# Performance work log

Hardware: AMD Instinct MI355X
Metric: run time of the kernel (lower is better)

## Reference

```python
import jax, jax.numpy as jnp
import numpy as np

D_MODEL = 1024
D_FF = 4096
NUM_EXPERTS = 8
TOP_K = 2
SEQ = 1024
BATCH = 2


def setup_inputs() -> dict:
    key = jax.random.key(0)
    ks = jax.random.split(key, 7)
    s = 0.02
    x = jax.random.normal(ks[0], (SEQ, BATCH, D_MODEL), dtype=jnp.float32)
    gate_w = jax.random.normal(ks[1], (D_MODEL, NUM_EXPERTS), dtype=jnp.float32) * s
    gate_b = jnp.zeros((NUM_EXPERTS,), dtype=jnp.float32)
    W1 = jax.random.normal(ks[2], (NUM_EXPERTS, D_MODEL, D_FF), dtype=jnp.float32) * s
    b1 = jnp.zeros((NUM_EXPERTS, D_FF), dtype=jnp.float32)
    W2 = jax.random.normal(ks[3], (NUM_EXPERTS, D_FF, D_MODEL), dtype=jnp.float32) * s
    b2 = jnp.zeros((NUM_EXPERTS, D_MODEL), dtype=jnp.float32)
    return {"x": x, "gate_w": gate_w, "gate_b": gate_b,
            "W1": W1, "b1": b1, "W2": W2, "b2": b2}


def reference(x, gate_w, gate_b, W1, b1, W2, b2):
    S, B, D = x.shape
    x_flat = x.reshape(-1, D)                       # [T, D], T = S*B
    scores = x_flat @ gate_w + gate_b               # [T, E]
    topk_vals, topk_idx = jax.lax.top_k(scores, TOP_K)   # [T, K]
    topk_probs = jax.nn.softmax(topk_vals, axis=-1)      # [T, K]
    # combine weight per (token, expert): sum of probs over slots routed to e
    one_hot = jax.nn.one_hot(topk_idx, NUM_EXPERTS, dtype=x.dtype)  # [T, K, E]
    combine = jnp.einsum('tk,tke->te', topk_probs, one_hot)         # [T, E]
    # dense per-expert FFN (tokens with combine weight 0 contribute nothing,
    # matching the masked gather/scatter in the torch loop)
    h = jax.nn.relu(jnp.einsum('td,edf->etf', x_flat, W1) + b1[:, None, :])  # [E, T, F]
    y = jnp.einsum('etf,efd->etd', h, W2) + b2[:, None, :]                    # [E, T, D]
    out = jnp.einsum('te,etd->td', combine, y)       # [T, D]
    return out.reshape(S, B, D)
```

## Files before the change

### kernel.cpp

```cpp
#include <hip/hip_runtime.h>
#include <stdint.h>

#define T_TOKENS 2048
#define DM 1024
#define DF 4096
#define NEXP 8
#define NSLOTS (T_TOKENS * 2)

typedef __bf16 bf16x8 __attribute__((ext_vector_type(8)));
typedef float f32x4 __attribute__((ext_vector_type(4)));

__device__ __forceinline__ ushort f2bf(float f) {
    union { float f; uint32_t u; } v; v.f = f;
    uint32_t r = v.u + 0x7FFFu + ((v.u >> 16) & 1u);
    return (ushort)(r >> 16);
}

__device__ __forceinline__ void gload16(const ushort* g, ushort* l) {
    __builtin_amdgcn_global_load_lds(
        (const __attribute__((address_space(1))) uint32_t*)g,
        (__attribute__((address_space(3))) uint32_t*)l,
        16, 0, 0);
}

__global__ void init_cnt(uint32_t* cnt) {
    if (threadIdx.x < NEXP) cnt[threadIdx.x] = 0;
}

__global__ __launch_bounds__(256) void gate_route(
    const float* __restrict__ x, const float* __restrict__ gw,
    const float* __restrict__ gb,
    uint32_t* __restrict__ route, uint32_t* __restrict__ cnt,
    float* __restrict__ prob)
{
    const int w = threadIdx.x >> 6;
    const int lane = threadIdx.x & 63;
    const int t = blockIdx.x * 4 + w;
    float acc[NEXP];
#pragma unroll
    for (int e = 0; e < NEXP; ++e) acc[e] = 0.f;
    const float* xr = x + (size_t)t * DM;
#pragma unroll
    for (int j = 0; j < DM / 64; ++j) {
        const int d = j * 64 + lane;
        const float xv = xr[d];
        const float* g = gw + (size_t)d * NEXP;
#pragma unroll
        for (int e = 0; e < NEXP; ++e) acc[e] += xv * g[e];
    }
#pragma unroll
    for (int e = 0; e < NEXP; ++e) {
#pragma unroll
        for (int off = 32; off > 0; off >>= 1)
            acc[e] += __shfl_xor(acc[e], off);
        acc[e] += gb[e];
    }
    if (lane == 0) {
        int e0 = 0; float v0 = acc[0];
#pragma unroll
        for (int e = 1; e < NEXP; ++e) if (acc[e] > v0) { v0 = acc[e]; e0 = e; }
        int e1 = -1; float v1 = -1e30f;
#pragma unroll
        for (int e = 0; e < NEXP; ++e) if (e != e0 && acc[e] > v1) { v1 = acc[e]; e1 = e; }
        const float ex = expf(v1 - v0);
        const float inv = 1.f / (1.f + ex);
        prob[t * 2 + 0] = inv;
        prob[t * 2 + 1] = ex * inv;
        uint32_t pos = atomicAdd(&cnt[e0], 1u);
        route[e0 * T_TOKENS + pos] = (uint32_t)(t * 2);
        pos = atomicAdd(&cnt[e1], 1u);
        route[e1 * T_TOKENS + pos] = (uint32_t)(t * 2 + 1);
    }
}

__global__ __launch_bounds__(256) void convert_x(const float* __restrict__ x,
                                                 ushort* __restrict__ xb)
{
    const int i = (blockIdx.x * 256 + threadIdx.x) * 4;
    const float4 v = *reinterpret_cast<const float4*>(x + i);
    ushort4 o;
    o.x = f2bf(v.x); o.y = f2bf(v.y); o.z = f2bf(v.z); o.w = f2bf(v.w);
    *reinterpret_cast<ushort4*>(xb + i) = o;
}

template<int K, int N>
__global__ __launch_bounds__(256) void conv_transpose(const float* __restrict__ W,
                                                      ushort* __restrict__ Wb)
{
    const int e  = blockIdx.y;
    const int nt = blockIdx.x % (N / 64);
    const int kt = blockIdx.x / (N / 64);
    const int k0 = kt * 64, n0 = nt * 64;
    __shared__ ushort T[64][80];
    const int t = threadIdx.x;
    const int kr = t >> 4, nc = (t & 15) * 4;
    const float* src = W + ((size_t)e * K + k0 + kr) * N + n0 + nc;
#pragma unroll
    for (int i = 0; i < 4; ++i) {
        const float4 v = *reinterpret_cast<const float4*>(src + (size_t)i * 16 * N);
        T[nc + 0][kr + i * 16] = f2bf(v.x);
        T[nc + 1][kr + i * 16] = f2bf(v.y);
        T[nc + 2][kr + i * 16] = f2bf(v.z);
        T[nc + 3][kr + i * 16] = f2bf(v.w);
    }
    __syncthreads();
    const int r = t >> 2, c0 = t & 3;
    ushort* dst = Wb + ((size_t)e * N + n0 + r) * K + k0;
#pragma unroll
    for (int i = 0; i < 2; ++i) {
        const int c = c0 + i * 4;
        const uint4 v = *reinterpret_cast<const uint4*>(&T[r][c * 8]);
        *reinterpret_cast<uint4*>(dst + c * 8) = v;
    }
}

template<int KD, int ND, bool FIRST, int SPLIT, int NT>
__global__ __launch_bounds__(256, 2) void moe_gemm4(
    const ushort* __restrict__ Abuf,
    const ushort* __restrict__ Wb,
    const float* __restrict__ bias,
    const uint32_t* __restrict__ route,
    const uint32_t* __restrict__ cnt,
    const float* __restrict__ prob,
    ushort* __restrict__ hout,
    float* __restrict__ yout)
{
    const int bx = blockIdx.x;
    const int e  = bx / (16 * NT);
    const int mt = (bx / NT) & 15;
    const int nt = bx % NT;
    const uint32_t cntE = cnt[e];
    const int m0 = mt * 128;
    if ((uint32_t)m0 >= cntE) return;
    const int n0 = nt * 128;
    const int z  = (SPLIT > 1) ? (int)blockIdx.z : 0;
    const int kbeg = z * (KD / SPLIT);
    const int niter = (KD / SPLIT) / 64;

    __shared__ ushort As[2][128 * 64];
    __shared__ ushort Bs[2][128 * 64];
    __shared__ uint32_t s_route[128];

    const int tid = threadIdx.x;
    if (tid < 128) {
        const uint32_t idx = (uint32_t)(m0 + tid);
        s_route[tid] = (idx < cntE) ? route[e * T_TOKENS + idx] : 0xFFFFFFFFu;
    }
    __syncthreads();

    const int w = tid >> 6, l = tid & 63;

    const ushort* asrc[4];
    const ushort* bsrc[4];
#pragma unroll
    for (int i = 0; i < 4; ++i) {
        const int chunk = (w * 4 + i) * 64 + l;
        const int row = chunk >> 3;
        const int c   = chunk & 7;
        const int cs  = c ^ (((row >> 2) & 1) << 1);
        const uint32_t s = s_route[row];
        const size_t ar = (s == 0xFFFFFFFFu) ? 0 : (FIRST ? (size_t)(s >> 1) : (size_t)s);
        asrc[i] = Abuf + ar * KD + cs * 8 + kbeg;
        bsrc[i] = Wb + ((size_t)e * ND + n0 + row) * KD + cs * 8 + kbeg;
    }

    f32x4 acc[4][4];
#pragma unroll
    for (int i = 0; i < 4; ++i)
#pragma unroll
        for (int j = 0; j < 4; ++j) acc[i][j] = (f32x4){0.f, 0.f, 0.f, 0.f};

    const int q = l & 15, g = l >> 4;
    const int wm = w >> 1, wn = w & 1;

    int aoff[4][2], boff[4][2];
#pragma unroll
    for (int mi = 0; mi < 4; ++mi)
#pragma unroll
        for (int ks = 0; ks < 2; ++ks) {
            int row = wm * 64 + mi * 16 + q;
            int b = row * 128 + ks * 64 + g * 16;
            b ^= ((b >> 9) & 1) << 5;
            aoff[mi][ks] = b;
            row = wn * 64 + mi * 16 + q;
            b = row * 128 + ks * 64 + g * 16;
            b ^= ((b >> 9) & 1) << 5;
            boff[mi][ks] = b;
        }

    ushort* const abase0 = &As[0][0];
    ushort* const bbase0 = &Bs[0][0];

#pragma unroll
    for (int i = 0; i < 4; ++i) gload16(asrc[i], abase0 + (w * 4 + i) * 512);
#pragma unroll
    for (int i = 0; i < 4; ++i) gload16(bsrc[i], bbase0 + (w * 4 + i) * 512);

    int cur = 0;
    for (int t = 0; t < niter; ++t) {
        if (t + 1 < niter) {
            ushort* ad = abase0 + (cur ^ 1) * (128 * 64) + (w * 4) * 512;
            ushort* bd = bbase0 + (cur ^ 1) * (128 * 64) + (w * 4) * 512;
            const int k1 = (t + 1) * 64;
#pragma unroll
            for (int i = 0; i < 4; ++i) gload16(asrc[i] + k1, ad + i * 512);
#pragma unroll
            for (int i = 0; i < 4; ++i) gload16(bsrc[i] + k1, bd + i * 512);
            asm volatile("s_waitcnt vmcnt(8)" ::: "memory");
        } else {
            asm volatile("s_waitcnt vmcnt(0)" ::: "memory");
        }
        __builtin_amdgcn_s_barrier();
        __builtin_amdgcn_sched_barrier(0);

        const char* Ab = (const char*)(abase0 + cur * (128 * 64));
        const char* Bb = (const char*)(bbase0 + cur * (128 * 64));
#pragma unroll
        for (int ks = 0; ks < 2; ++ks) {
            bf16x8 af[4], bv[4];
#pragma unroll
            for (int mi = 0; mi < 4; ++mi)
                af[mi] = *reinterpret_cast<const bf16x8*>(Ab + aoff[mi][ks]);
#pragma unroll
            for (int ni = 0; ni < 4; ++ni)
                bv[ni] = *reinterpret_cast<const bf16x8*>(Bb + boff[ni][ks]);
            __builtin_amdgcn_s_setprio(1);
#pragma unroll
            for (int mi = 0; mi < 4; ++mi)
#pragma unroll
                for (int ni = 0; ni < 4; ++ni)
                    acc[mi][ni] = __builtin_amdgcn_mfma_f32_16x16x32_bf16(
                        af[mi], bv[ni], acc[mi][ni], 0, 0, 0);
            __builtin_amdgcn_s_setprio(0);
        }
        __builtin_amdgcn_s_barrier();
        cur ^= 1;
    }

    const float* brow = bias + (size_t)e * ND;
#pragma unroll
    for (int mi = 0; mi < 4; ++mi) {
#pragma unroll
        for (int ni = 0; ni < 4; ++ni) {
            const int gcol = n0 + wn * 64 + ni * 16 + q;
            const float bv = (SPLIT == 1 || z == 0) ? brow[gcol] : 0.f;
#pragma unroll
            for (int j = 0; j < 4; ++j) {
                const int row = wm * 64 + mi * 16 + g * 4 + j;
                if ((uint32_t)(m0 + row) < cntE) {
                    const uint32_t s = s_route[row];
                    float v = acc[mi][ni][j] + bv;
                    if (FIRST) {
                        v = fmaxf(v, 0.f);
                        hout[(size_t)s * ND + gcol] = f2bf(v);
                    } else {
                        yout[((size_t)z * NSLOTS + s) * ND + gcol] = v * prob[s];
                    }
                }
            }
        }
    }
}

__global__ __launch_bounds__(256) void combine2(const float* __restrict__ yc,
                                                float* __restrict__ out)
{
    const int gid = blockIdx.x * 256 + threadIdx.x;
    const int t = gid >> 8;
    const int dq = gid & 255;
    const float4* Y = reinterpret_cast<const float4*>(yc);
    const float4 a = Y[(size_t)(2 * t) * 256 + dq];
    const float4 b = Y[(size_t)(2 * t + 1) * 256 + dq];
    const float4 c = Y[((size_t)NSLOTS + 2 * t) * 256 + dq];
    const float4 d = Y[((size_t)NSLOTS + 2 * t + 1) * 256 + dq];
    const float4 o = { a.x + b.x + c.x + d.x, a.y + b.y + c.y + d.y,
                       a.z + b.z + c.z + d.z, a.w + b.w + c.w + d.w };
    reinterpret_cast<float4*>(out)[gid] = o;
}

template<int KD, int ND, bool FIRST>
__global__ __launch_bounds__(256) void moe_gemm_v1(
    const ushort* __restrict__ Abuf, const float* __restrict__ W,
    const float* __restrict__ bias, const uint32_t* __restrict__ route,
    const uint32_t* __restrict__ cnt, const float* __restrict__ prob,
    ushort* __restrict__ hout, float* __restrict__ yout)
{
    const int e = blockIdx.x >> 4;
    const int mt = blockIdx.x & 15;
    const uint32_t cntE = cnt[e];
    const int m0 = mt * 128;
    if ((uint32_t)m0 >= cntE) return;
    const int n0 = blockIdx.y * 128;
    const int tid = threadIdx.x;
    __shared__ ushort Asm[128][40];
    __shared__ ushort Bsm[128][40];
    __shared__ uint32_t s_route[128];
    if (tid < 128) {
        const uint32_t idx = (uint32_t)(m0 + tid);
        s_route[tid] = (idx < cntE) ? route[e * T_TOKENS + idx] : 0xFFFFFFFFu;
    }
    __syncthreads();
    const int ar = tid >> 1, ah = tid & 1;
    const uint32_t s_a = s_route[ar];
    size_t arow = 0;
    if (s_a != 0xFFFFFFFFu) arow = FIRST ? (size_t)(s_a >> 1) : (size_t)s_a;
    const ushort* asrc = Abuf + arow * KD + ah * 16;
    const int c4 = tid & 31, kq = tid >> 5;
    const float* wbase = W + (size_t)e * KD * ND + (size_t)n0 + (size_t)c4 * 4;
    f32x4 acc[4][4];
#pragma unroll
    for (int i = 0; i < 4; ++i)
#pragma unroll
        for (int j = 0; j < 4; ++j) acc[i][j] = (f32x4){0.f, 0.f, 0.f, 0.f};
    const int lane = tid & 63, wv = tid >> 6;
    const int wm = wv >> 1, wn = wv & 1;
    const int q = lane & 15, g = lane >> 4;
    for (int k0 = 0; k0 < KD; k0 += 32) {
        {
            const uint4* src = reinterpret_cast<const uint4*>(asrc + k0);
            const uint4 v0 = src[0];
            const uint4 v1 = src[1];
            *reinterpret_cast<uint4*>(&Asm[ar][ah * 16]) = v0;
            *reinterpret_cast<uint4*>(&Asm[ar][ah * 16 + 8]) = v1;
        }
        {
            ushort vals[4][4];
#pragma unroll
            for (int r = 0; r < 4; ++r) {
                const float4 v = *reinterpret_cast<const float4*>(
                    wbase + (size_t)(k0 + kq * 4 + r) * ND);
                vals[r][0] = f2bf(v.x); vals[r][1] = f2bf(v.y);
                vals[r][2] = f2bf(v.z); vals[r][3] = f2bf(v.w);
            }
#pragma unroll
            for (int c = 0; c < 4; ++c) {
                const ushort4 o = { vals[0][c], vals[1][c], vals[2][c], vals[3][c] };
                *reinterpret_cast<ushort4*>(&Bsm[c4 * 4 + c][kq * 4]) = o;
            }
        }
        __syncthreads();
        bf16x8 af[4], bfr[4];
#pragma unroll
        for (int mi = 0; mi < 4; ++mi)
            af[mi] = *reinterpret_cast<const bf16x8*>(&Asm[wm * 64 + mi * 16 + q][g * 8]);
#pragma unroll
        for (int ni = 0; ni < 4; ++ni)
            bfr[ni] = *reinterpret_cast<const bf16x8*>(&Bsm[wn * 64 + ni * 16 + q][g * 8]);
#pragma unroll
        for (int mi = 0; mi < 4; ++mi)
#pragma unroll
            for (int ni = 0; ni < 4; ++ni)
                acc[mi][ni] = __builtin_amdgcn_mfma_f32_16x16x32_bf16(
                    af[mi], bfr[ni], acc[mi][ni], 0, 0, 0);
        __syncthreads();
    }
#pragma unroll
    for (int mi = 0; mi < 4; ++mi) {
#pragma unroll
        for (int ni = 0; ni < 4; ++ni) {
            const int gcol = n0 + wn * 64 + ni * 16 + q;
#pragma unroll
            for (int j = 0; j < 4; ++j) {
                const int row = wm * 64 + mi * 16 + g * 4 + j;
                if ((uint32_t)(m0 + row) < cntE) {
                    const uint32_t s = s_route[row];
                    float v = acc[mi][ni][j] + bias[e * ND + gcol];
                    if (FIRST) {
                        v = fmaxf(v, 0.f);
                        hout[(size_t)s * ND + gcol] = f2bf(v);
                    } else {
                        yout[(size_t)s * ND + gcol] = v * prob[s];
                    }
                }
            }
        }
    }
}

__global__ __launch_bounds__(256) void combine1(const float* __restrict__ yc,
                                                float* __restrict__ out)
{
    const int gid = blockIdx.x * 256 + threadIdx.x;
    const int t = gid >> 8;
    const int dq = gid & 255;
    const float4 va = reinterpret_cast<const float4*>(yc)[(size_t)(2 * t) * 256 + dq];
    const float4 vb = reinterpret_cast<const float4*>(yc)[(size_t)(2 * t + 1) * 256 + dq];
    const float4 o = { va.x + vb.x, va.y + vb.y, va.z + vb.z, va.w + vb.w };
    reinterpret_cast<float4*>(out)[gid] = o;
}

extern "C" void kernel_launch(void* const* d_in, const int* in_sizes, int n_in,
                              void* d_out, int out_size, void* d_ws, size_t ws_size,
                              hipStream_t stream)
{
    const float* x  = (const float*)d_in[0];
    const float* gw = (const float*)d_in[1];
    const float* gb = (const float*)d_in[2];
    const float* W1 = (const float*)d_in[3];
    const float* b1 = (const float*)d_in[4];
    const float* W2 = (const float*)d_in[5];
    const float* b2 = (const float*)d_in[6];
    float* out = (float*)d_out;
    char* ws = (char*)d_ws;

    const size_t OFF_XB    = 0;
    const size_t OFF_H     = 4194304;
    const size_t OFF_YC    = 37748736;
    const size_t OFF_ROUTE = 71303168;
    const size_t OFF_CNT   = 71368704;
    const size_t OFF_PROB  = 71368768;
    const size_t OFF_W1B   = 71385152;
    const size_t OFF_W2B   = 138494016;
    const size_t NEED      = 205602880ull;

    if (ws_size >= NEED) {
        ushort*   xb    = (ushort*)(ws + OFF_XB);
        ushort*   h     = (ushort*)(ws + OFF_H);
        float*    yc    = (float*)(ws + OFF_YC);
        uint32_t* route = (uint32_t*)(ws + OFF_ROUTE);
        uint32_t* cnt   = (uint32_t*)(ws + OFF_CNT);
        float*    prob  = (float*)(ws + OFF_PROB);
        ushort*   w1b   = (ushort*)(ws + OFF_W1B);
        ushort*   w2b   = (ushort*)(ws + OFF_W2B);

        hipLaunchKernelGGL(init_cnt, dim3(1), dim3(64), 0, stream, cnt);
        hipLaunchKernelGGL(gate_route, dim3(T_TOKENS / 4), dim3(256), 0, stream,
                           x, gw, gb, route, cnt, prob);
        hipLaunchKernelGGL(convert_x, dim3(T_TOKENS * DM / 1024), dim3(256), 0, stream, x, xb);
        hipLaunchKernelGGL((conv_transpose<DM, DF>), dim3((DM / 64) * (DF / 64), NEXP),
                           dim3(256), 0, stream, W1, w1b);
        hipLaunchKernelGGL((conv_transpose<DF, DM>), dim3((DF / 64) * (DM / 64), NEXP),
                           dim3(256), 0, stream, W2, w2b);
        hipLaunchKernelGGL((moe_gemm4<DM, DF, true, 1, 32>),
                           dim3(NEXP * 16 * 32, 1, 1), dim3(256), 0, stream,
                           xb, w1b, b1, route, cnt, prob, h, (float*)nullptr);
        hipLaunchKernelGGL((moe_gemm4<DF, DM, false, 2, 8>),
                           dim3(NEXP * 16 * 8, 1, 2), dim3(256), 0, stream,
                           h, w2b, b2, route, cnt, prob, (ushort*)nullptr, yc);
        hipLaunchKernelGGL(combine2, dim3(T_TOKENS * DM / 1024), dim3(256), 0, stream, yc, out);
    } else {
        const size_t F_XB = 0, F_H = 4194304, F_YC = 37748736;
        const size_t F_ROUTE = 54525952, F_CNT = 54591488, F_PROB = 54591552;
        ushort*   xb    = (ushort*)(ws + F_XB);
        ushort*   h     = (ushort*)(ws + F_H);
        float*    yc    = (float*)(ws + F_YC);
        uint32_t* route = (uint32_t*)(ws + F_ROUTE);
        uint32_t* cnt   = (uint32_t*)(ws + F_CNT);
        float*    prob  = (float*)(ws + F_PROB);

        hipLaunchKernelGGL(init_cnt, dim3(1), dim3(64), 0, stream, cnt);
        hipLaunchKernelGGL(gate_route, dim3(T_TOKENS / 4), dim3(256), 0, stream,
                           x, gw, gb, route, cnt, prob);
        hipLaunchKernelGGL(convert_x, dim3(T_TOKENS * DM / 1024), dim3(256), 0, stream, x, xb);
        hipLaunchKernelGGL((moe_gemm_v1<DM, DF, true>), dim3(NEXP * 16, DF / 128),
                           dim3(256), 0, stream, xb, W1, b1, route, cnt, prob,
                           h, (float*)nullptr);
        hipLaunchKernelGGL((moe_gemm_v1<DF, DM, false>), dim3(NEXP * 16, DM / 128),
                           dim3(256), 0, stream, h, W2, b2, route, cnt, prob,
                           (ushort*)nullptr, yc);
        hipLaunchKernelGGL(combine1, dim3(T_TOKENS * DM / 1024), dim3(256), 0, stream, yc, out);
    }
}
```

Measured before the change: 334.7 us.

## Halve GEMM K-tile for higher occupancy and use four-way split-K

The MoE GEMM K-tile drops from 64 to 32, halving shared memory per block. The launch bound rises to 4 blocks per SM so more waves can hide load latency. The second GEMM now splits K four ways instead of two, and the combine kernel sums four partial buffers per slot. To fit the larger partial buffer, it reuses the W1 bf16 region, which is dead after the first GEMM. The cost is twice as many barriers per MFMA and twice the partial-sum traffic written and read back.

After: 315.7 us. 5.7% less time.

```diff
diff --git a/kernel.cpp b/kernel.cpp
--- a/kernel.cpp
+++ b/kernel.cpp
@@ -115,7 +115,7 @@
 }
 
 template<int KD, int ND, bool FIRST, int SPLIT, int NT>
-__global__ __launch_bounds__(256, 2) void moe_gemm4(
+__global__ __launch_bounds__(256, 4) void moe_gemm5(
     const ushort* __restrict__ Abuf,
     const ushort* __restrict__ Wb,
     const float* __restrict__ bias,
@@ -135,10 +135,10 @@
     const int n0 = nt * 128;
     const int z  = (SPLIT > 1) ? (int)blockIdx.z : 0;
     const int kbeg = z * (KD / SPLIT);
-    const int niter = (KD / SPLIT) / 64;
-
-    __shared__ ushort As[2][128 * 64];
-    __shared__ ushort Bs[2][128 * 64];
+    const int niter = (KD / SPLIT) / 32;
+
+    __shared__ ushort As[2][128 * 32];
+    __shared__ ushort Bs[2][128 * 32];
     __shared__ uint32_t s_route[128];
 
     const int tid = threadIdx.x;
@@ -150,14 +150,14 @@
 
     const int w = tid >> 6, l = tid & 63;
 
-    const ushort* asrc[4];
-    const ushort* bsrc[4];
-#pragma unroll
-    for (int i = 0; i < 4; ++i) {
-        const int chunk = (w * 4 + i) * 64 + l;
-        const int row = chunk >> 3;
-        const int c   = chunk & 7;
-        const int cs  = c ^ (((row >> 2) & 1) << 1);
+    const ushort* asrc[2];
+    const ushort* bsrc[2];
+#pragma unroll
+    for (int i = 0; i < 2; ++i) {
+        const int chunk = (w * 2 + i) * 64 + l;
+        const int row = chunk >> 2;
+        const int c   = chunk & 3;
+        const int cs  = c ^ ((row >> 1) & 3);
         const uint32_t s = s_route[row];
         const size_t ar = (s == 0xFFFFFFFFu) ? 0 : (FIRST ? (size_t)(s >> 1) : (size_t)s);
         asrc[i] = Abuf + ar * KD + cs * 8 + kbeg;
@@ -173,66 +173,57 @@
     const int q = l & 15, g = l >> 4;
     const int wm = w >> 1, wn = w & 1;
 
-    int aoff[4][2], boff[4][2];
-#pragma unroll
-    for (int mi = 0; mi < 4; ++mi)
-#pragma unroll
-        for (int ks = 0; ks < 2; ++ks) {
-            int row = wm * 64 + mi * 16 + q;
-            int b = row * 128 + ks * 64 + g * 16;
-            b ^= ((b >> 9) & 1) << 5;
-            aoff[mi][ks] = b;
-            row = wn * 64 + mi * 16 + q;
-            b = row * 128 + ks * 64 + g * 16;
-            b ^= ((b >> 9) & 1) << 5;
-            boff[mi][ks] = b;
-        }
+    int aoff[4], boff[4];
+#pragma unroll
+    for (int mi = 0; mi < 4; ++mi) {
+        int row = wm * 64 + mi * 16 + q;
+        aoff[mi] = row * 64 + (g ^ ((row >> 1) & 3)) * 16;
+        row = wn * 64 + mi * 16 + q;
+        boff[mi] = row * 64 + (g ^ ((row >> 1) & 3)) * 16;
+    }
 
     ushort* const abase0 = &As[0][0];
     ushort* const bbase0 = &Bs[0][0];
 
 #pragma unroll
-    for (int i = 0; i < 4; ++i) gload16(asrc[i], abase0 + (w * 4 + i) * 512);
-#pragma unroll
-    for (int i = 0; i < 4; ++i) gload16(bsrc[i], bbase0 + (w * 4 + i) * 512);
+    for (int i = 0; i < 2; ++i) gload16(asrc[i], abase0 + (w * 2 + i) * 512);
+#pragma unroll
+    for (int i = 0; i < 2; ++i) gload16(bsrc[i], bbase0 + (w * 2 + i) * 512);
 
     int cur = 0;
     for (int t = 0; t < niter; ++t) {
         if (t + 1 < niter) {
-            ushort* ad = abase0 + (cur ^ 1) * (128 * 64) + (w * 4) * 512;
-            ushort* bd = bbase0 + (cur ^ 1) * (128 * 64) + (w * 4) * 512;
-            const int k1 = (t + 1) * 64;
-#pragma unroll
-            for (int i = 0; i < 4; ++i) gload16(asrc[i] + k1, ad + i * 512);
-#pragma unroll
-            for (int i = 0; i < 4; ++i) gload16(bsrc[i] + k1, bd + i * 512);
-            asm volatile("s_waitcnt vmcnt(8)" ::: "memory");
+            ushort* ad = abase0 + (cur ^ 1) * (128 * 32) + (w * 2) * 512;
+            ushort* bd = bbase0 + (cur ^ 1) * (128 * 32) + (w * 2) * 512;
+            const int k1 = (t + 1) * 32;
+#pragma unroll
+            for (int i = 0; i < 2; ++i) gload16(asrc[i] + k1, ad + i * 512);
+#pragma unroll
+            for (int i = 0; i < 2; ++i) gload16(bsrc[i] + k1, bd + i * 512);
+            asm volatile("s_waitcnt vmcnt(4)" ::: "memory");
         } else {
             asm volatile("s_waitcnt vmcnt(0)" ::: "memory");
         }
         __builtin_amdgcn_s_barrier();
         __builtin_amdgcn_sched_barrier(0);
 
-        const char* Ab = (const char*)(abase0 + cur * (128 * 64));
-        const char* Bb = (const char*)(bbase0 + cur * (128 * 64));
-#pragma unroll
-        for (int ks = 0; ks < 2; ++ks) {
-            bf16x8 af[4], bv[4];
-#pragma unroll
-            for (int mi = 0; mi < 4; ++mi)
-                af[mi] = *reinterpret_cast<const bf16x8*>(Ab + aoff[mi][ks]);
+        const char* Ab = (const char*)(abase0 + cur * (128 * 32));
+        const char* Bb = (const char*)(bbase0 + cur * (128 * 32));
+        bf16x8 af[4], bv[4];
+#pragma unroll
+        for (int mi = 0; mi < 4; ++mi)
+            af[mi] = *reinterpret_cast<const bf16x8*>(Ab + aoff[mi]);
+#pragma unroll
+        for (int ni = 0; ni < 4; ++ni)
+            bv[ni] = *reinterpret_cast<const bf16x8*>(Bb + boff[ni]);
+        __builtin_amdgcn_s_setprio(1);
+#pragma unroll
+        for (int mi = 0; mi < 4; ++mi)
 #pragma unroll
             for (int ni = 0; ni < 4; ++ni)
-                bv[ni] = *reinterpret_cast<const bf16x8*>(Bb + boff[ni][ks]);
-            __builtin_amdgcn_s_setprio(1);
-#pragma unroll
-            for (int mi = 0; mi < 4; ++mi)
-#pragma unroll
-                for (int ni = 0; ni < 4; ++ni)
-                    acc[mi][ni] = __builtin_amdgcn_mfma_f32_16x16x32_bf16(
-                        af[mi], bv[ni], acc[mi][ni], 0, 0, 0);
-            __builtin_amdgcn_s_setprio(0);
-        }
+                acc[mi][ni] = __builtin_amdgcn_mfma_f32_16x16x32_bf16(
+                    af[mi], bv[ni], acc[mi][ni], 0, 0, 0);
+        __builtin_amdgcn_s_setprio(0);
         __builtin_amdgcn_s_barrier();
         cur ^= 1;
     }
@@ -262,19 +253,22 @@
     }
 }
 
-__global__ __launch_bounds__(256) void combine2(const float* __restrict__ yc,
+__global__ __launch_bounds__(256) void combine4(const float* __restrict__ yc,
                                                 float* __restrict__ out)
 {
     const int gid = blockIdx.x * 256 + threadIdx.x;
     const int t = gid >> 8;
     const int dq = gid & 255;
     const float4* Y = reinterpret_cast<const float4*>(yc);
-    const float4 a = Y[(size_t)(2 * t) * 256 + dq];
-    const float4 b = Y[(size_t)(2 * t + 1) * 256 + dq];
-    const float4 c = Y[((size_t)NSLOTS + 2 * t) * 256 + dq];
-    const float4 d = Y[((size_t)NSLOTS + 2 * t + 1) * 256 + dq];
-    const float4 o = { a.x + b.x + c.x + d.x, a.y + b.y + c.y + d.y,
-                       a.z + b.z + c.z + d.z, a.w + b.w + c.w + d.w };
+    float4 o = {0.f, 0.f, 0.f, 0.f};
+#pragma unroll
+    for (int zz = 0; zz < 4; ++zz) {
+#pragma unroll
+        for (int k = 0; k < 2; ++k) {
+            const float4 v = Y[((size_t)zz * NSLOTS + 2 * t + k) * 256 + dq];
+            o.x += v.x; o.y += v.y; o.z += v.z; o.w += v.w;
+        }
+    }
     reinterpret_cast<float4*>(out)[gid] = o;
 }
 
@@ -405,13 +399,13 @@
 
     const size_t OFF_XB    = 0;
     const size_t OFF_H     = 4194304;
-    const size_t OFF_YC    = 37748736;
-    const size_t OFF_ROUTE = 71303168;
-    const size_t OFF_CNT   = 71368704;
-    const size_t OFF_PROB  = 71368768;
-    const size_t OFF_W1B   = 71385152;
-    const size_t OFF_W2B   = 138494016;
-    const size_t NEED      = 205602880ull;
+    const size_t OFF_ROUTE = 37748736;
+    const size_t OFF_CNT   = 37814272;
+    const size_t OFF_PROB  = 37814336;
+    const size_t OFF_W1B   = 38797312;
+    const size_t OFF_W2B   = 105906176;
+    const size_t OFF_YC    = OFF_W1B;
+    const size_t NEED      = 173015040ull;
 
     if (ws_size >= NEED) {
         ushort*   xb    = (ushort*)(ws + OFF_XB);
@@ -431,13 +425,13 @@
                            dim3(256), 0, stream, W1, w1b);
         hipLaunchKernelGGL((conv_transpose<DF, DM>), dim3((DF / 64) * (DM / 64), NEXP),
                            dim3(256), 0, stream, W2, w2b);
-        hipLaunchKernelGGL((moe_gemm4<DM, DF, true, 1, 32>),
+        hipLaunchKernelGGL((moe_gemm5<DM, DF, true, 1, 32>),
                            dim3(NEXP * 16 * 32, 1, 1), dim3(256), 0, stream,
                            xb, w1b, b1, route, cnt, prob, h, (float*)nullptr);
-        hipLaunchKernelGGL((moe_gemm4<DF, DM, false, 2, 8>),
-                           dim3(NEXP * 16 * 8, 1, 2), dim3(256), 0, stream,
+        hipLaunchKernelGGL((moe_gemm5<DF, DM, false, 4, 8>),
+                           dim3(NEXP * 16 * 8, 1, 4), dim3(256), 0, stream,
                            h, w2b, b2, route, cnt, prob, (ushort*)nullptr, yc);
-        hipLaunchKernelGGL(combine2, dim3(T_TOKENS * DM / 1024), dim3(256), 0, stream, yc, out);
+        hipLaunchKernelGGL(combine4, dim3(T_TOKENS * DM / 1024), dim3(256), 0, stream, yc, out);
     } else {
         const size_t F_XB = 0, F_H = 4194304, F_YC = 37748736;
         const size_t F_ROUTE = 54525952, F_CNT = 54591488, F_PROB = 54591552;
```
